# Kernel optimization log

Measured on AMD Instinct MI355X. Metric: run time of the kernel, lower is better.

The kernel has to match this reference:

```python
import jax, jax.numpy as jnp
import numpy as np

# Model/config constants (match init_kwargs)
B, S, D, H = 2, 2048, 512, 8
HD = D // H            # head dim = 64
WIN, DIL, G = 16, 2, 64  # window size, dilation rate, num global tokens
L = S - G              # 1984 local tokens (global indices are 0..G-1)


def setup_inputs() -> dict:
    key = jax.random.key(0)
    ks = jax.random.split(key, 16)
    sc = 0.02
    n = jax.random.normal
    return {
        "query": n(ks[0], (B, S, D), jnp.float32),
        "key": n(ks[1], (B, S, D), jnp.float32),
        "value": n(ks[2], (B, S, D), jnp.float32),
        # local multi-head attention params (linear_query/key/value/out_proj)
        "wq": n(ks[3], (D, D), jnp.float32) * sc, "bq": jnp.zeros((D,), jnp.float32),
        "wk": n(ks[4], (D, D), jnp.float32) * sc, "bk": jnp.zeros((D,), jnp.float32),
        "wv": n(ks[5], (D, D), jnp.float32) * sc, "bv": jnp.zeros((D,), jnp.float32),
        "wo": n(ks[6], (D, D), jnp.float32) * sc, "bo": jnp.zeros((D,), jnp.float32),
        # global nn.MultiheadAttention params (packed in_proj + out_proj)
        "g_in_w": n(ks[7], (3 * D, D), jnp.float32) * sc,
        "g_in_b": jnp.zeros((3 * D,), jnp.float32),
        "g_out_w": n(ks[8], (D, D), jnp.float32) * sc,
        "g_out_b": jnp.zeros((D,), jnp.float32),
    }


def _window_indices():
    # centered dilated window per local position, clipped to valid range
    pos = jnp.arange(L)
    offs = DIL * (jnp.arange(WIN) - WIN // 2)
    return jnp.clip(pos[:, None] + offs[None, :], 0, L - 1)


def reference(query, key, value, wq, bq, wk, bk, wv, bv, wo, bo,
              g_in_w, g_in_b, g_out_w, g_out_b):
    scale = 1.0 / np.sqrt(HD).astype(np.float32)

    # ---- local (dilated sliding window) path over tokens G..S-1 ----
    q_loc = query[:, G:, :]                      # (B, L, D)
    widx = _window_indices()
    k_win = key[:, G:, :][:, widx, :]
    v_win = value[:, G:, :][:, widx, :]

    q = (q_loc @ wq.T + bq).reshape(B, L, H, HD)          # (B,L,H,HD)
    k = (k_win @ wk.T + bk).reshape(B, L, WIN, H, HD)     # (B,L,W,H,HD)
    v = (v_win @ wv.T + bv).reshape(B, L, WIN, H, HD)

    scores = jnp.einsum('blhd,blwhd->blhw', q, k) * scale
    p = jax.nn.softmax(scores, axis=-1)
    o = jnp.einsum('blhw,blwhd->blhd', p, v).reshape(B, L, D)
    local_out = o @ wo.T + bo                              # (B,L,D)

    # ---- global token path: standard MHA over the G global tokens ----
    wq_g, wk_g, wv_g = g_in_w[:D], g_in_w[D:2 * D], g_in_w[2 * D:]
    bq_g, bk_g, bv_g = g_in_b[:D], g_in_b[D:2 * D], g_in_b[2 * D:]
    qg = (query[:, :G] @ wq_g.T + bq_g).reshape(B, G, H, HD)
    kg = (key[:, :G] @ wk_g.T + bk_g).reshape(B, G, H, HD)
    vg = (value[:, :G] @ wv_g.T + bv_g).reshape(B, G, H, HD)
    sg = jnp.einsum('bqhd,bkhd->bhqk', qg, kg) * scale     # (B,H,G,G)
    pg = jax.nn.softmax(sg, axis=-1)
    og = jnp.einsum('bhqk,bkhd->bqhd', pg, vg).reshape(B, G, D)
    global_out = og @ g_out_w.T + g_out_b                  # (B,G,D)

    # ---- fuse: scatter local + global back into full sequence ----
    out = jnp.zeros((B, S, D), query.dtype)
    out = out.at[:, G:, :].set(local_out)
    out = out.at[:, :G, :].set(global_out)
    return out
```

## Files before the change

kernel.cpp:

```cpp
#include <hip/hip_runtime.h>
#include <stdint.h>

#define B_ 2
#define S_ 2048
#define D_ 512
#define H_ 8
#define WIN_ 16
#define DIL_ 2
#define G_ 64
#define L_ (S_ - G_)

typedef short bf16x8 __attribute__((ext_vector_type(8)));
typedef float f32x4 __attribute__((ext_vector_type(4)));
typedef unsigned short u16;

__device__ __forceinline__ float bf2f(u16 h) {
  return __uint_as_float(((uint32_t)h) << 16);
}
__device__ __forceinline__ u16 f2bf(float f) {
  uint32_t u = __float_as_uint(f);
  uint32_t r = (u + 0x7fffu + ((u >> 16) & 1u)) >> 16;
  return (u16)r;
}

__device__ __forceinline__ void gload16(const u16* g, u16* l) {
  __builtin_amdgcn_global_load_lds(
      (const __attribute__((address_space(1))) void*)g,
      (__attribute__((address_space(3))) void*)l, 16, 0, 0);
}

struct CvtJob { const float* src; u16* dst; int n4; };
struct CvtArgs { CvtJob job[9]; };

__global__ __launch_bounds__(256) void cvt_kernel(CvtArgs a) {
  CvtJob j = a.job[blockIdx.y];
  int stride = gridDim.x * blockDim.x;
  for (int i = blockIdx.x * blockDim.x + threadIdx.x; i < j.n4; i += stride) {
    float4 v = reinterpret_cast<const float4*>(j.src)[i];
    ushort4 o;
    o.x = f2bf(v.x); o.y = f2bf(v.y); o.z = f2bf(v.z); o.w = f2bf(v.w);
    reinterpret_cast<ushort4*>(j.dst)[i] = o;
  }
}

struct Job {
  const u16* X; const u16* W; const float* bias; void* Y;
  int rpb;
  int xoff;
  long xbs;
  int yoff;
  long ybs;
  int out_f32;
};
struct GemmLaunch { int start[6]; Job job[6]; };

__global__ __launch_bounds__(256) void gemm_kernel(GemmLaunch a) {
  int j = 0;
#pragma unroll
  for (int i = 1; i < 6; ++i) j = ((int)blockIdx.x >= a.start[i]) ? i : j;
  const Job jb = a.job[j];
  const int bid = blockIdx.x - a.start[j];
  const int tm = bid >> 3, tn = bid & 7;
  const int row0 = tm * 128, n0 = tn * 64;

  __shared__ __align__(16) u16 As[128 * 32];
  __shared__ __align__(16) u16 Bs[64 * 32];

  const int tid = threadIdx.x, lane = tid & 63, w = tid >> 6;
  const int wm = w >> 1, wn = w & 1;

  const int rA = w * 16 + (lane >> 2);
  const int kq = (lane & 3) * 8;

  const int ra0 = row0 + rA,        ba0 = ra0 >= jb.rpb;
  const int ra1 = row0 + 64 + rA,   ba1 = ra1 >= jb.rpb;
  const u16* xa0 = jb.X + (size_t)(ba0 ? jb.xbs : 0) +
                   (size_t)(jb.xoff + ra0 - (ba0 ? jb.rpb : 0)) * 512 + kq;
  const u16* xa1 = jb.X + (size_t)(ba1 ? jb.xbs : 0) +
                   (size_t)(jb.xoff + ra1 - (ba1 ? jb.rpb : 0)) * 512 + kq;
  const u16* wb  = jb.W + (size_t)(n0 + rA) * 512 + kq;
  u16* la0 = As + w * 512;
  u16* la1 = As + 2048 + w * 512;
  u16* lb  = Bs + w * 512;

  f32x4 acc[4][2];
#pragma unroll
  for (int i = 0; i < 4; ++i)
#pragma unroll
    for (int k = 0; k < 2; ++k) acc[i][k] = (f32x4){0.f, 0.f, 0.f, 0.f};

  for (int kt = 0; kt < 16; ++kt) {
    gload16(xa0, la0);
    gload16(xa1, la1);
    gload16(wb,  lb);
    xa0 += 32; xa1 += 32; wb += 32;
    __syncthreads();

    bf16x8 af[4], bfr[2];
#pragma unroll
    for (int fm = 0; fm < 4; ++fm)
      af[fm] = *(const bf16x8*)&As[(wm * 64 + fm * 16 + (lane & 15)) * 32 + 8 * (lane >> 4)];
#pragma unroll
    for (int fn = 0; fn < 2; ++fn)
      bfr[fn] = *(const bf16x8*)&Bs[(wn * 32 + fn * 16 + (lane & 15)) * 32 + 8 * (lane >> 4)];
#pragma unroll
    for (int fm = 0; fm < 4; ++fm)
#pragma unroll
      for (int fn = 0; fn < 2; ++fn)
        acc[fm][fn] = __builtin_amdgcn_mfma_f32_16x16x32_bf16(af[fm], bfr[fn], acc[fm][fn], 0, 0, 0);
    __syncthreads();
  }

#pragma unroll
  for (int fm = 0; fm < 4; ++fm) {
#pragma unroll
    for (int fn = 0; fn < 2; ++fn) {
#pragma unroll
      for (int r = 0; r < 4; ++r) {
        const int row = row0 + wm * 64 + fm * 16 + (lane >> 4) * 4 + r;
        const int col = n0 + wn * 32 + fn * 16 + (lane & 15);
        const int b = row >= jb.rpb;
        const int rr = row - (b ? jb.rpb : 0);
        const size_t yi = (size_t)(b ? jb.ybs : 0) + (size_t)(jb.yoff + rr) * 512 + col;
        const float v = acc[fm][fn][r] + jb.bias[col];
        if (jb.out_f32) ((float*)jb.Y)[yi] = v;
        else            ((u16*)jb.Y)[yi]   = f2bf(v);
      }
    }
  }
}

__global__ __launch_bounds__(256) void attn_kernel(const u16* qp, const u16* kp,
                                                   const u16* vp, u16* ob,
                                                   const u16* qgp, const u16* kgp,
                                                   const u16* vgp, u16* ogp) {
  const int lane = threadIdx.x & 63;
  const int wid = blockIdx.x * 4 + (threadIdx.x >> 6);

  if (wid < B_ * L_) {
    const int l = wid % L_;
    const int brow = wid - l;
    float q[8];
    {
      bf16x8 qv = *(const bf16x8*)&qp[(size_t)wid * 512 + lane * 8];
#pragma unroll
      for (int e = 0; e < 8; ++e) q[e] = bf2f((u16)qv[e]);
    }
    float s[WIN_];
#pragma unroll
    for (int w2 = 0; w2 < WIN_; ++w2) {
      int ki = l + DIL_ * w2 - WIN_;
      ki = ki < 0 ? 0 : (ki > L_ - 1 ? L_ - 1 : ki);
      bf16x8 kv = *(const bf16x8*)&kp[(size_t)(brow + ki) * 512 + lane * 8];
      float p = 0.f;
#pragma unroll
      for (int e = 0; e < 8; ++e) p = fmaf(q[e], bf2f((u16)kv[e]), p);
      p += __shfl_xor(p, 1); p += __shfl_xor(p, 2); p += __shfl_xor(p, 4);
      s[w2] = p * 0.125f;
    }
    float m = s[0];
#pragma unroll
    for (int w2 = 1; w2 < WIN_; ++w2) m = fmaxf(m, s[w2]);
    float sum = 0.f;
#pragma unroll
    for (int w2 = 0; w2 < WIN_; ++w2) { s[w2] = __expf(s[w2] - m); sum += s[w2]; }
    const float inv = 1.0f / sum;
    float acc[8] = {0.f};
#pragma unroll
    for (int w2 = 0; w2 < WIN_; ++w2) {
      int ki = l + DIL_ * w2 - WIN_;
      ki = ki < 0 ? 0 : (ki > L_ - 1 ? L_ - 1 : ki);
      bf16x8 vv = *(const bf16x8*)&vp[(size_t)(brow + ki) * 512 + lane * 8];
#pragma unroll
      for (int e = 0; e < 8; ++e) acc[e] = fmaf(s[w2], bf2f((u16)vv[e]), acc[e]);
    }
    bf16x8 o8;
#pragma unroll
    for (int e = 0; e < 8; ++e) o8[e] = (short)f2bf(acc[e] * inv);
    *(bf16x8*)&ob[(size_t)wid * 512 + lane * 8] = o8;
  } else {
    const int g = wid - B_ * L_;
    const int base = (g >> 6) * 64;
    const int qi = g & 63;
    float q[8];
    {
      bf16x8 qv = *(const bf16x8*)&qgp[(size_t)(base + qi) * 512 + lane * 8];
#pragma unroll
      for (int e = 0; e < 8; ++e) q[e] = bf2f((u16)qv[e]);
    }
    float m = -1e30f, sum = 0.f, acc[8] = {0.f};
    for (int j2 = 0; j2 < 64; ++j2) {
      bf16x8 kv = *(const bf16x8*)&kgp[(size_t)(base + j2) * 512 + lane * 8];
      float p = 0.f;
#pragma unroll
      for (int e = 0; e < 8; ++e) p = fmaf(q[e], bf2f((u16)kv[e]), p);
      p += __shfl_xor(p, 1); p += __shfl_xor(p, 2); p += __shfl_xor(p, 4);
      p *= 0.125f;
      const float mn = fmaxf(m, p);
      const float c  = __expf(m - mn);
      const float pe = __expf(p - mn);
      sum = sum * c + pe;
      m = mn;
      bf16x8 vv = *(const bf16x8*)&vgp[(size_t)(base + j2) * 512 + lane * 8];
#pragma unroll
      for (int e = 0; e < 8; ++e) acc[e] = fmaf(acc[e], c, 0.f) + pe * bf2f((u16)vv[e]);
    }
    const float inv = 1.0f / sum;
    bf16x8 o8;
#pragma unroll
    for (int e = 0; e < 8; ++e) o8[e] = (short)f2bf(acc[e] * inv);
    *(bf16x8*)&ogp[(size_t)(base + qi) * 512 + lane * 8] = o8;
  }
}

extern "C" void kernel_launch(void* const* d_in, const int* in_sizes, int n_in,
                              void* d_out, int out_size, void* d_ws, size_t ws_size,
                              hipStream_t stream) {
  const float* query   = (const float*)d_in[0];
  const float* key     = (const float*)d_in[1];
  const float* value   = (const float*)d_in[2];
  const float* wq      = (const float*)d_in[3];
  const float* bq      = (const float*)d_in[4];
  const float* wk      = (const float*)d_in[5];
  const float* bk      = (const float*)d_in[6];
  const float* wv      = (const float*)d_in[7];
  const float* bv      = (const float*)d_in[8];
  const float* wo      = (const float*)d_in[9];
  const float* bo      = (const float*)d_in[10];
  const float* g_in_w  = (const float*)d_in[11];
  const float* g_in_b  = (const float*)d_in[12];
  const float* g_out_w = (const float*)d_in[13];
  const float* g_out_b = (const float*)d_in[14];
  float* out = (float*)d_out;

  u16* w16 = (u16*)d_ws;
  const size_t QKV = (size_t)B_ * S_ * D_;
  const size_t WSZ = (size_t)D_ * D_;
  const size_t PSZ = (size_t)B_ * L_ * D_;
  const size_t GSZ = (size_t)B_ * G_ * D_;

  u16* qb  = w16;              u16* kb  = qb + QKV;   u16* vb  = kb + QKV;
  u16* wqb = vb + QKV;         u16* wkb = wqb + WSZ;  u16* wvb = wkb + WSZ;
  u16* wob = wvb + WSZ;
  u16* gqw = wob + WSZ;        u16* gkw = gqw + WSZ;  u16* gvw = gkw + WSZ;
  u16* gow = gvw + WSZ;
  u16* qp  = gow + WSZ;        u16* kp  = qp + PSZ;   u16* vp  = kp + PSZ;
  u16* ob  = vp + PSZ;
  u16* qgp = ob + PSZ;         u16* kgp = qgp + GSZ;  u16* vgp = kgp + GSZ;
  u16* ogp = vgp + GSZ;

  CvtArgs ca;
  ca.job[0] = {query, qb, (int)(QKV / 4)};
  ca.job[1] = {key,   kb, (int)(QKV / 4)};
  ca.job[2] = {value, vb, (int)(QKV / 4)};
  ca.job[3] = {wq, wqb, (int)(WSZ / 4)};
  ca.job[4] = {wk, wkb, (int)(WSZ / 4)};
  ca.job[5] = {wv, wvb, (int)(WSZ / 4)};
  ca.job[6] = {wo, wob, (int)(WSZ / 4)};
  ca.job[7] = {g_in_w, gqw, (int)(3 * WSZ / 4)};
  ca.job[8] = {g_out_w, gow, (int)(WSZ / 4)};
  hipLaunchKernelGGL(cvt_kernel, dim3(512, 9), dim3(256), 0, stream, ca);

  const long XBS = (long)S_ * D_;
  const long PBS = (long)L_ * D_;
  const long GBS = (long)G_ * D_;

  GemmLaunch gi;
  gi.start[0] = 0; gi.start[1] = 248; gi.start[2] = 496;
  gi.start[3] = 744; gi.start[4] = 752; gi.start[5] = 760;
  gi.job[0] = {qb, wqb, bq, qp, L_, G_, XBS, 0, PBS, 0};
  gi.job[1] = {kb, wkb, bk, kp, L_, G_, XBS, 0, PBS, 0};
  gi.job[2] = {vb, wvb, bv, vp, L_, G_, XBS, 0, PBS, 0};
  gi.job[3] = {qb, gqw, g_in_b,           qgp, G_, 0, XBS, 0, GBS, 0};
  gi.job[4] = {kb, gkw, g_in_b + D_,      kgp, G_, 0, XBS, 0, GBS, 0};
  gi.job[5] = {vb, gvw, g_in_b + 2 * D_,  vgp, G_, 0, XBS, 0, GBS, 0};
  hipLaunchKernelGGL(gemm_kernel, dim3(768), dim3(256), 0, stream, gi);

  hipLaunchKernelGGL(attn_kernel, dim3((B_ * L_ + 128) / 4), dim3(256), 0, stream,
                     qp, kp, vp, ob, qgp, kgp, vgp, ogp);

  GemmLaunch go;
  go.start[0] = 0; go.start[1] = 248;
  go.start[2] = go.start[3] = go.start[4] = go.start[5] = 0x7fffffff;
  go.job[0] = {ob,  wob, bo,      out, L_, 0, PBS, G_, XBS, 1};
  go.job[1] = {ogp, gow, g_out_b, out, G_, 0, GBS, 0,  XBS, 1};
  go.job[2] = go.job[0]; go.job[3] = go.job[0]; go.job[4] = go.job[0]; go.job[5] = go.job[0];
  hipLaunchKernelGGL(gemm_kernel, dim3(256), dim3(256), 0, stream, go);
}
```

Measured before the change: 177.5 us.

## Enlarge GEMM tiles to 128x128 with double-buffered LDS and XCD-aware block remap

The GEMM kernel moves from 128x64 to 128x128 output tiles, so each wave computes a 4x4 grid of MFMA fragments. LDS is now double-buffered so the next K-slice loads while the current one computes, removing one barrier per iteration. Block indices in both GEMM and attention are remapped so consecutive blocks land on the same XCD, aiming for better L2 locality. The trade-off is that the grids shrink to 384 and 128 blocks, which lowers occupancy and parallelism on a 256-CU part and raises register use.

```diff
diff --git a/kernel.cpp b/kernel.cpp
--- a/kernel.cpp
+++ b/kernel.cpp
@@ -55,70 +55,81 @@
 struct GemmLaunch { int start[6]; Job job[6]; };
 
 __global__ __launch_bounds__(256) void gemm_kernel(GemmLaunch a) {
+  int bid = (int)blockIdx.x;
+  bid = (bid & 7) * ((int)gridDim.x >> 3) + (bid >> 3);
+
   int j = 0;
 #pragma unroll
-  for (int i = 1; i < 6; ++i) j = ((int)blockIdx.x >= a.start[i]) ? i : j;
+  for (int i = 1; i < 6; ++i) j = (bid >= a.start[i]) ? i : j;
   const Job jb = a.job[j];
-  const int bid = blockIdx.x - a.start[j];
-  const int tm = bid >> 3, tn = bid & 7;
-  const int row0 = tm * 128, n0 = tn * 64;
-
-  __shared__ __align__(16) u16 As[128 * 32];
-  __shared__ __align__(16) u16 Bs[64 * 32];
+  bid -= a.start[j];
+  const int tm = bid >> 2, tn = bid & 3;
+  const int row0 = tm * 128, n0 = tn * 128;
+
+  __shared__ __align__(16) u16 As[2][128 * 32];
+  __shared__ __align__(16) u16 Bs[2][128 * 32];
 
   const int tid = threadIdx.x, lane = tid & 63, w = tid >> 6;
   const int wm = w >> 1, wn = w & 1;
 
-  const int rA = w * 16 + (lane >> 2);
-  const int kq = (lane & 3) * 8;
-
-  const int ra0 = row0 + rA,        ba0 = ra0 >= jb.rpb;
-  const int ra1 = row0 + 64 + rA,   ba1 = ra1 >= jb.rpb;
-  const u16* xa0 = jb.X + (size_t)(ba0 ? jb.xbs : 0) +
-                   (size_t)(jb.xoff + ra0 - (ba0 ? jb.rpb : 0)) * 512 + kq;
-  const u16* xa1 = jb.X + (size_t)(ba1 ? jb.xbs : 0) +
-                   (size_t)(jb.xoff + ra1 - (ba1 ? jb.rpb : 0)) * 512 + kq;
-  const u16* wb  = jb.W + (size_t)(n0 + rA) * 512 + kq;
-  u16* la0 = As + w * 512;
-  u16* la1 = As + 2048 + w * 512;
-  u16* lb  = Bs + w * 512;
-
-  f32x4 acc[4][2];
+  const int rA = tid >> 2;
+  const int kq = (tid & 3) * 8;
+
+  const int r0 = row0 + rA,      b0 = r0 >= jb.rpb;
+  const int r1 = row0 + 64 + rA, b1 = r1 >= jb.rpb;
+  const u16* xa0 = jb.X + (size_t)(b0 ? jb.xbs : 0) +
+                   (size_t)(jb.xoff + r0 - (b0 ? jb.rpb : 0)) * 512 + kq;
+  const u16* xa1 = jb.X + (size_t)(b1 ? jb.xbs : 0) +
+                   (size_t)(jb.xoff + r1 - (b1 ? jb.rpb : 0)) * 512 + kq;
+  const u16* wb0 = jb.W + (size_t)(n0 + rA) * 512 + kq;
+  const u16* wb1 = jb.W + (size_t)(n0 + 64 + rA) * 512 + kq;
+
+  f32x4 acc[4][4];
 #pragma unroll
   for (int i = 0; i < 4; ++i)
 #pragma unroll
-    for (int k = 0; k < 2; ++k) acc[i][k] = (f32x4){0.f, 0.f, 0.f, 0.f};
-
-  for (int kt = 0; kt < 16; ++kt) {
-    gload16(xa0, la0);
-    gload16(xa1, la1);
-    gload16(wb,  lb);
-    xa0 += 32; xa1 += 32; wb += 32;
+    for (int k = 0; k < 4; ++k) acc[i][k] = (f32x4){0.f, 0.f, 0.f, 0.f};
+
+  auto stage = [&](int buf, int kof) {
+    gload16(xa0 + kof, &As[buf][w * 512]);
+    gload16(xa1 + kof, &As[buf][2048 + w * 512]);
+    gload16(wb0 + kof, &Bs[buf][w * 512]);
+    gload16(wb1 + kof, &Bs[buf][2048 + w * 512]);
+  };
+  auto compute = [&](int buf) {
+    bf16x8 af[4], bfv[4];
+#pragma unroll
+    for (int fm = 0; fm < 4; ++fm)
+      af[fm] = *(const bf16x8*)&As[buf][(wm * 64 + fm * 16 + (lane & 15)) * 32 + 8 * (lane >> 4)];
+#pragma unroll
+    for (int fn = 0; fn < 4; ++fn)
+      bfv[fn] = *(const bf16x8*)&Bs[buf][(wn * 64 + fn * 16 + (lane & 15)) * 32 + 8 * (lane >> 4)];
+#pragma unroll
+    for (int fm = 0; fm < 4; ++fm)
+#pragma unroll
+      for (int fn = 0; fn < 4; ++fn)
+        acc[fm][fn] = __builtin_amdgcn_mfma_f32_16x16x32_bf16(af[fm], bfv[fn], acc[fm][fn], 0, 0, 0);
+  };
+
+  stage(0, 0);
+  __syncthreads();
+  int cur = 0;
+  for (int kt = 0; kt < 15; ++kt) {
+    stage(cur ^ 1, (kt + 1) * 32);
+    compute(cur);
     __syncthreads();
-
-    bf16x8 af[4], bfr[2];
-#pragma unroll
-    for (int fm = 0; fm < 4; ++fm)
-      af[fm] = *(const bf16x8*)&As[(wm * 64 + fm * 16 + (lane & 15)) * 32 + 8 * (lane >> 4)];
-#pragma unroll
-    for (int fn = 0; fn < 2; ++fn)
-      bfr[fn] = *(const bf16x8*)&Bs[(wn * 32 + fn * 16 + (lane & 15)) * 32 + 8 * (lane >> 4)];
-#pragma unroll
-    for (int fm = 0; fm < 4; ++fm)
-#pragma unroll
-      for (int fn = 0; fn < 2; ++fn)
-        acc[fm][fn] = __builtin_amdgcn_mfma_f32_16x16x32_bf16(af[fm], bfr[fn], acc[fm][fn], 0, 0, 0);
-    __syncthreads();
+    cur ^= 1;
   }
+  compute(cur);
 
 #pragma unroll
   for (int fm = 0; fm < 4; ++fm) {
 #pragma unroll
-    for (int fn = 0; fn < 2; ++fn) {
+    for (int fn = 0; fn < 4; ++fn) {
 #pragma unroll
       for (int r = 0; r < 4; ++r) {
         const int row = row0 + wm * 64 + fm * 16 + (lane >> 4) * 4 + r;
-        const int col = n0 + wn * 32 + fn * 16 + (lane & 15);
+        const int col = n0 + wn * 64 + fn * 16 + (lane & 15);
         const int b = row >= jb.rpb;
         const int rr = row - (b ? jb.rpb : 0);
         const size_t yi = (size_t)(b ? jb.ybs : 0) + (size_t)(jb.yoff + rr) * 512 + col;
@@ -135,7 +146,10 @@
                                                    const u16* qgp, const u16* kgp,
                                                    const u16* vgp, u16* ogp) {
   const int lane = threadIdx.x & 63;
-  const int wid = blockIdx.x * 4 + (threadIdx.x >> 6);
+  int bid = (int)blockIdx.x;
+  const int nbl = (B_ * L_) / 4;
+  if (bid < nbl) bid = (bid & 7) * (nbl >> 3) + (bid >> 3);
+  const int wid = bid * 4 + (threadIdx.x >> 6);
 
   if (wid < B_ * L_) {
     const int l = wid % L_;
@@ -203,7 +217,7 @@
       m = mn;
       bf16x8 vv = *(const bf16x8*)&vgp[(size_t)(base + j2) * 512 + lane * 8];
 #pragma unroll
-      for (int e = 0; e < 8; ++e) acc[e] = fmaf(acc[e], c, 0.f) + pe * bf2f((u16)vv[e]);
+      for (int e = 0; e < 8; ++e) acc[e] = acc[e] * c + pe * bf2f((u16)vv[e]);
     }
     const float inv = 1.0f / sum;
     bf16x8 o8;
@@ -266,24 +280,24 @@
   const long GBS = (long)G_ * D_;
 
   GemmLaunch gi;
-  gi.start[0] = 0; gi.start[1] = 248; gi.start[2] = 496;
-  gi.start[3] = 744; gi.start[4] = 752; gi.start[5] = 760;
+  gi.start[0] = 0; gi.start[1] = 124; gi.start[2] = 248;
+  gi.start[3] = 372; gi.start[4] = 376; gi.start[5] = 380;
   gi.job[0] = {qb, wqb, bq, qp, L_, G_, XBS, 0, PBS, 0};
   gi.job[1] = {kb, wkb, bk, kp, L_, G_, XBS, 0, PBS, 0};
   gi.job[2] = {vb, wvb, bv, vp, L_, G_, XBS, 0, PBS, 0};
   gi.job[3] = {qb, gqw, g_in_b,           qgp, G_, 0, XBS, 0, GBS, 0};
   gi.job[4] = {kb, gkw, g_in_b + D_,      kgp, G_, 0, XBS, 0, GBS, 0};
   gi.job[5] = {vb, gvw, g_in_b + 2 * D_,  vgp, G_, 0, XBS, 0, GBS, 0};
-  hipLaunchKernelGGL(gemm_kernel, dim3(768), dim3(256), 0, stream, gi);
+  hipLaunchKernelGGL(gemm_kernel, dim3(384), dim3(256), 0, stream, gi);
 
   hipLaunchKernelGGL(attn_kernel, dim3((B_ * L_ + 128) / 4), dim3(256), 0, stream,
                      qp, kp, vp, ob, qgp, kgp, vgp, ogp);
 
   GemmLaunch go;
-  go.start[0] = 0; go.start[1] = 248;
+  go.start[0] = 0; go.start[1] = 124;
   go.start[2] = go.start[3] = go.start[4] = go.start[5] = 0x7fffffff;
   go.job[0] = {ob,  wob, bo,      out, L_, 0, PBS, G_, XBS, 1};
   go.job[1] = {ogp, gow, g_out_b, out, G_, 0, GBS, 0,  XBS, 1};
-  go.job[2] = go.job[0]; go.job[3] = go.job[0]; go.job[4] = go.job[0]; go.job[5] = go.job[0];
-  hipLaunchKernelGGL(gemm_kernel, dim3(256), dim3(256), 0, stream, go);
-}
+  go.job[2] = go.job[1]; go.job[3] = go.job[1]; go.job[4] = go.job[1]; go.job[5] = go.job[1];
+  hipLaunchKernelGGL(gemm_kernel, dim3(128), dim3(256), 0, stream, go);
+}
```

Measured after the change: 181.6 us. 2.3% more time.
